# Kernel optimization log

Hardware: AMD Instinct MI355X
Metric: run time of the kernel (lower is better)

Reference implementation:

```python
import jax, jax.numpy as jnp
import numpy as np

N_NODES = 100000
N_EDGES = 1600000
IN_DIM, HID_DIM, N_CLASSES = 128, 64, 40


def spmm(edge_row, edge_col, edge_val, dense):
    # sparse [N,N] @ dense [N,D] via gather + segment-sum over edges
    msgs = edge_val[:, None] * dense[edge_col]            # [E, D]
    return jax.ops.segment_sum(msgs, edge_row, num_segments=N_NODES)


def setup_inputs() -> dict:
    key = jax.random.key(0)
    ks = jax.random.split(key, 8)
    x = jax.random.normal(ks[0], (N_NODES, IN_DIM), dtype=jnp.float32)
    edge_row = jax.random.randint(ks[1], (N_EDGES,), 0, N_NODES, dtype=jnp.int32)
    edge_col = jax.random.randint(ks[2], (N_EDGES,), 0, N_NODES, dtype=jnp.int32)
    edge_val = jax.random.uniform(ks[3], (N_EDGES,), dtype=jnp.float32)
    s1 = 1.0 / np.sqrt(IN_DIM)
    s2 = 1.0 / np.sqrt(HID_DIM)
    W1 = jax.random.normal(ks[4], (IN_DIM, HID_DIM), dtype=jnp.float32) * s1
    b1 = jnp.zeros((HID_DIM,), dtype=jnp.float32)
    W2 = jax.random.normal(ks[5], (HID_DIM, HID_DIM), dtype=jnp.float32) * s2
    b2 = jnp.zeros((HID_DIM,), dtype=jnp.float32)
    Wc = jax.random.normal(ks[6], (HID_DIM, N_CLASSES), dtype=jnp.float32) * s2
    bc = jnp.zeros((N_CLASSES,), dtype=jnp.float32)
    return {"x": x, "edge_row": edge_row, "edge_col": edge_col, "edge_val": edge_val,
            "W1": W1, "b1": b1, "W2": W2, "b2": b2, "Wc": Wc, "bc": bc}


def reference(x, edge_row, edge_col, edge_val, W1, b1, W2, b2, Wc, bc):
    # GCN layer 1: support = xW+b, aggregate, relu  (dropout off in eval)
    h = jax.nn.relu(spmm(edge_row, edge_col, edge_val, x @ W1 + b1))
    # GCN layer 2
    h = spmm(edge_row, edge_col, edge_val, h @ W2 + b2)
    # node classifier + log-softmax
    logits = h @ Wc + bc
    return jax.nn.log_softmax(logits, axis=-1)
```

## Files before the change

### kernel.cpp

```cpp
#include <hip/hip_runtime.h>

#define N_NODES   100000
#define N_EDGES   1600000
#define IN_DIM    128
#define HID_DIM   64
#define N_CLASSES 40

#define NBUCK 782
#define BCAP  2816
#define EPB   6400
#define PBLK  1024
#define GRID_A 250

typedef __attribute__((ext_vector_type(8))) short bf16x8;
typedef __attribute__((ext_vector_type(4))) float f32x4;

__device__ inline short f2bf(float f) {
    unsigned u = __float_as_uint(f);
    unsigned r = (u + 0x7FFFu + ((u >> 16) & 1u)) >> 16;
    return (short)r;
}
__device__ inline float bflo(unsigned w) { return __uint_as_float(w << 16); }
__device__ inline float bfhi(unsigned w) { return __uint_as_float(w & 0xFFFF0000u); }
__device__ inline float upval(unsigned w) { return __uint_as_float((w >> 17) << 16); }

__global__ __launch_bounds__(PBLK) void prep_parta(const int* __restrict__ erow,
                                                   const int* __restrict__ ecol,
                                                   const float* __restrict__ eval,
                                                   int* __restrict__ bcnt,
                                                   int2* __restrict__ tmp,
                                                   const float* __restrict__ W1,
                                                   const float* __restrict__ W2,
                                                   const float* __restrict__ Wc,
                                                   const float* __restrict__ b2,
                                                   short* __restrict__ W1t,
                                                   short* __restrict__ Mt,
                                                   float* __restrict__ bv) {
    __shared__ int2 pay[EPB];
    __shared__ int hist[NBUCK], lbase[NBUCK], cur[NBUCK], dofs[NBUCK], scan[NBUCK];
    int tid = threadIdx.x;
    if (blockIdx.x >= GRID_A) {
        int pb = blockIdx.x - GRID_A;
        {
            int i = pb * PBLK + tid;
            int n = i >> 7, k = i & 127;
            W1t[i] = f2bf(W1[k * HID_DIM + n]);
        }
        if (pb == 0) {
            for (int idx = tid; idx < HID_DIM * HID_DIM; idx += PBLK) {
                int n = idx >> 6, i = idx & 63;
                float acc = 0.f;
                if (n < N_CLASSES)
                    for (int j = 0; j < HID_DIM; ++j)
                        acc = fmaf(W2[i * HID_DIM + j], Wc[j * N_CLASSES + n], acc);
                Mt[n * HID_DIM + i] = f2bf(acc);
            }
        }
        if (pb == 1 && tid < N_CLASSES) {
            float acc = 0.f;
            for (int j = 0; j < HID_DIM; ++j)
                acc = fmaf(b2[j], Wc[j * N_CLASSES + tid], acc);
            bv[tid] = acc;
        }
        return;
    }
    int e0 = blockIdx.x * EPB;
    for (int i = tid; i < NBUCK; i += PBLK) { hist[i] = 0; cur[i] = 0; }
    __syncthreads();
    for (int i = tid; i < EPB; i += PBLK)
        atomicAdd(&hist[erow[e0 + i] >> 7], 1);
    __syncthreads();
    for (int i = tid; i < NBUCK; i += PBLK) {
        int n = hist[i];
        dofs[i] = i * BCAP + (n ? atomicAdd(&bcnt[i], n) : 0);
        scan[i] = n;
    }
    __syncthreads();
    for (int off = 1; off < NBUCK; off <<= 1) {
        int t = 0;
        if (tid < NBUCK && tid >= off) t = scan[tid - off];
        __syncthreads();
        if (tid < NBUCK) scan[tid] += t;
        __syncthreads();
    }
    if (tid < NBUCK) {
        lbase[tid] = scan[tid] - hist[tid];
        dofs[tid] -= lbase[tid];
    }
    __syncthreads();
    for (int i = tid; i < EPB; i += PBLK) {
        int e = e0 + i;
        int r = erow[e];
        int b = r >> 7;
        int p = lbase[b] + atomicAdd(&cur[b], 1);
        unsigned u = __float_as_uint(eval[e]);
        unsigned vb = ((u + 0x7FFFu + ((u >> 16) & 1u)) >> 16) & 0x7FFFu;
        pay[p] = make_int2(((r & 127) << 17) | ecol[e], (int)((vb << 10) | (unsigned)b));
    }
    __syncthreads();
    for (int p = tid; p < EPB; p += PBLK) {
        int2 v = pay[p];
        int b = (unsigned)v.y & 1023u;
        int dest = dofs[b] + p;
        if (dest < (b + 1) * BCAP)
            tmp[dest] = v;
    }
}

__global__ __launch_bounds__(256) void part_b_gemm1(const int* __restrict__ bcnt,
                                                    const int2* __restrict__ tmp,
                                                    unsigned* __restrict__ tmp2,
                                                    int2* __restrict__ rowmeta,
                                                    const float* __restrict__ x,
                                                    const short* __restrict__ W1t,
                                                    const float* __restrict__ b1,
                                                    unsigned short* __restrict__ outH) {
    __shared__ int2 ein[BCAP];
    __shared__ unsigned eout[BCAP];
    __shared__ int hist[128], pad[128], basep[128], cur[128], scan[128];
    if (blockIdx.x < NBUCK) {
        int b = blockIdx.x;
        int nb = bcnt[b]; if (nb > BCAP) nb = BCAP;
        for (int i = threadIdx.x; i < nb; i += 256) ein[i] = tmp[(size_t)b * BCAP + i];
        if (threadIdx.x < 128) { hist[threadIdx.x] = 0; cur[threadIdx.x] = 0; }
        __syncthreads();
        for (int i = threadIdx.x; i < nb; i += 256)
            atomicAdd(&hist[(ein[i].x >> 17) & 127], 1);
        __syncthreads();
        if (threadIdx.x < 128) {
            pad[threadIdx.x] = (hist[threadIdx.x] + 3) & ~3;
            scan[threadIdx.x] = pad[threadIdx.x];
        }
        __syncthreads();
        for (int off = 1; off < 128; off <<= 1) {
            int t = 0;
            if (threadIdx.x < 128 && threadIdx.x >= off) t = scan[threadIdx.x - off];
            __syncthreads();
            if (threadIdx.x < 128) scan[threadIdx.x] += t;
            __syncthreads();
        }
        if (threadIdx.x < 128) basep[threadIdx.x] = scan[threadIdx.x] - pad[threadIdx.x];
        __syncthreads();
        int ntot = scan[127]; if (ntot > BCAP) ntot = BCAP;
        for (int i = threadIdx.x; i < nb; i += 256) {
            int lr = (ein[i].x >> 17) & 127;
            int p = basep[lr] + atomicAdd(&cur[lr], 1);
            if (p < BCAP) {
                unsigned vb = ((unsigned)ein[i].y >> 10) & 0x7FFFu;
                eout[p] = (vb << 17) | (unsigned)(ein[i].x & 0x1FFFF);
            }
        }
        __syncthreads();
        if (threadIdx.x < 128) {
            int pe = basep[threadIdx.x] + pad[threadIdx.x];
            for (int p = basep[threadIdx.x] + hist[threadIdx.x]; p < pe && p < BCAP; ++p)
                eout[p] = 0u;
        }
        __syncthreads();
        for (int i = threadIdx.x; i < ntot; i += 256) tmp2[(size_t)b * BCAP + i] = eout[i];
        if (threadIdx.x < 128) {
            int r = b * 128 + threadIdx.x;
            if (r < N_NODES)
                rowmeta[r] = make_int2(b * BCAP + basep[threadIdx.x], pad[threadIdx.x]);
        }
    } else {
        int gb = blockIdx.x - NBUCK;
        int wave = threadIdx.x >> 6;
        int lane = threadIdx.x & 63;
        int node0 = gb * 64 + wave * 16;
        if (node0 >= N_NODES) return;
        int m = lane & 15;
        int q = lane >> 4;
        const float* xrow = x + (size_t)(node0 + m) * IN_DIM;
        f32x4 acc0 = {0,0,0,0}, acc1 = {0,0,0,0}, acc2 = {0,0,0,0}, acc3 = {0,0,0,0};
#pragma unroll
        for (int kb = 0; kb < 4; ++kb) {
            int k0 = kb * 32 + q * 8;
            float4 a0 = *(const float4*)(xrow + k0);
            float4 a1 = *(const float4*)(xrow + k0 + 4);
            bf16x8 af;
            af[0]=f2bf(a0.x); af[1]=f2bf(a0.y); af[2]=f2bf(a0.z); af[3]=f2bf(a0.w);
            af[4]=f2bf(a1.x); af[5]=f2bf(a1.y); af[6]=f2bf(a1.z); af[7]=f2bf(a1.w);
            bf16x8 bf0 = *(const bf16x8*)(W1t + ( 0 + m) * IN_DIM + k0);
            bf16x8 bf1 = *(const bf16x8*)(W1t + (16 + m) * IN_DIM + k0);
            bf16x8 bf2 = *(const bf16x8*)(W1t + (32 + m) * IN_DIM + k0);
            bf16x8 bf3 = *(const bf16x8*)(W1t + (48 + m) * IN_DIM + k0);
            acc0 = __builtin_amdgcn_mfma_f32_16x16x32_bf16(af, bf0, acc0, 0, 0, 0);
            acc1 = __builtin_amdgcn_mfma_f32_16x16x32_bf16(af, bf1, acc1, 0, 0, 0);
            acc2 = __builtin_amdgcn_mfma_f32_16x16x32_bf16(af, bf2, acc2, 0, 0, 0);
            acc3 = __builtin_amdgcn_mfma_f32_16x16x32_bf16(af, bf3, acc3, 0, 0, 0);
        }
        f32x4 accs[4] = {acc0, acc1, acc2, acc3};
#pragma unroll
        for (int t = 0; t < 4; ++t) {
            float bias = b1[t * 16 + m];
#pragma unroll
            for (int r = 0; r < 4; ++r) {
                int node = node0 + q * 4 + r;
                outH[(size_t)node * HID_DIM + t * 16 + m] = (unsigned short)f2bf(accs[t][r] + bias);
            }
        }
    }
}

__global__ __launch_bounds__(256) void spmm1_mm(const int2* __restrict__ rowmeta,
                                                const unsigned* __restrict__ ecv,
                                                const unsigned short* __restrict__ dense,
                                                const short* __restrict__ Mt,
                                                unsigned short* __restrict__ outU) {
    __shared__ unsigned lm[4][8][68];
    __shared__ unsigned short tr[32][64];
    int wave = threadIdx.x >> 6;
    int lane = threadIdx.x & 63;
    int s = lane >> 3, dq = lane & 7;
    int row = wave * 8 + s;
    int r = blockIdx.x * 32 + row;
    int2 meta = rowmeta[r];
    int beg = meta.x, deg = meta.y;
    int degc = deg < 64 ? deg : 64;
    for (int e = dq; e < degc; e += 8)
        lm[wave][s][e] = ecv[beg + e];
    __syncthreads();
    const unsigned* mp = lm[wave][s];
    float a0=0,a1=0,a2=0,a3=0,a4=0,a5=0,a6=0,a7=0;
    if (deg > 0) {
        uint4 w = *(const uint4*)mp;
        for (int e = 0; e < degc; e += 4) {
            uint4 wn = (e + 4 < degc) ? *(const uint4*)(mp + e + 4) : w;
            uint4 g0 = *(const uint4*)(dense + ((size_t)(w.x & 0x1FFFF) << 6) + (dq << 3));
            uint4 g1 = *(const uint4*)(dense + ((size_t)(w.y & 0x1FFFF) << 6) + (dq << 3));
            uint4 g2 = *(const uint4*)(dense + ((size_t)(w.z & 0x1FFFF) << 6) + (dq << 3));
            uint4 g3 = *(const uint4*)(dense + ((size_t)(w.w & 0x1FFFF) << 6) + (dq << 3));
            float v0 = upval(w.x), v1 = upval(w.y), v2 = upval(w.z), v3 = upval(w.w);
            a0=fmaf(v0,bflo(g0.x),a0); a1=fmaf(v0,bfhi(g0.x),a1); a2=fmaf(v0,bflo(g0.y),a2); a3=fmaf(v0,bfhi(g0.y),a3);
            a4=fmaf(v0,bflo(g0.z),a4); a5=fmaf(v0,bfhi(g0.z),a5); a6=fmaf(v0,bflo(g0.w),a6); a7=fmaf(v0,bfhi(g0.w),a7);
            a0=fmaf(v1,bflo(g1.x),a0); a1=fmaf(v1,bfhi(g1.x),a1); a2=fmaf(v1,bflo(g1.y),a2); a3=fmaf(v1,bfhi(g1.y),a3);
            a4=fmaf(v1,bflo(g1.z),a4); a5=fmaf(v1,bfhi(g1.z),a5); a6=fmaf(v1,bflo(g1.w),a6); a7=fmaf(v1,bfhi(g1.w),a7);
            a0=fmaf(v2,bflo(g2.x),a0); a1=fmaf(v2,bfhi(g2.x),a1); a2=fmaf(v2,bflo(g2.y),a2); a3=fmaf(v2,bfhi(g2.y),a3);
            a4=fmaf(v2,bflo(g2.z),a4); a5=fmaf(v2,bfhi(g2.z),a5); a6=fmaf(v2,bflo(g2.w),a6); a7=fmaf(v2,bfhi(g2.w),a7);
            a0=fmaf(v3,bflo(g3.x),a0); a1=fmaf(v3,bfhi(g3.x),a1); a2=fmaf(v3,bflo(g3.y),a2); a3=fmaf(v3,bfhi(g3.y),a3);
            a4=fmaf(v3,bflo(g3.z),a4); a5=fmaf(v3,bfhi(g3.z),a5); a6=fmaf(v3,bflo(g3.w),a6); a7=fmaf(v3,bfhi(g3.w),a7);
            w = wn;
        }
        for (int e = 64; e < deg; ++e) {
            unsigned we = ecv[beg + e];
            uint4 g = *(const uint4*)(dense + ((size_t)(we & 0x1FFFF) << 6) + (dq << 3));
            float v = upval(we);
            a0=fmaf(v,bflo(g.x),a0); a1=fmaf(v,bfhi(g.x),a1); a2=fmaf(v,bflo(g.y),a2); a3=fmaf(v,bfhi(g.y),a3);
            a4=fmaf(v,bflo(g.z),a4); a5=fmaf(v,bfhi(g.z),a5); a6=fmaf(v,bflo(g.w),a6); a7=fmaf(v,bfhi(g.w),a7);
        }
    }
    uint4 o;
    o.x = (unsigned short)f2bf(fmaxf(a0,0.f)) | ((unsigned)(unsigned short)f2bf(fmaxf(a1,0.f)) << 16);
    o.y = (unsigned short)f2bf(fmaxf(a2,0.f)) | ((unsigned)(unsigned short)f2bf(fmaxf(a3,0.f)) << 16);
    o.z = (unsigned short)f2bf(fmaxf(a4,0.f)) | ((unsigned)(unsigned short)f2bf(fmaxf(a5,0.f)) << 16);
    o.w = (unsigned short)f2bf(fmaxf(a6,0.f)) | ((unsigned)(unsigned short)f2bf(fmaxf(a7,0.f)) << 16);
    *(uint4*)(&tr[row][(dq ^ s) << 3]) = o;
    __syncthreads();
    int m = lane & 15;
    int q = lane >> 4;
    int nt = wave >> 1;
    int tb = (wave & 1) << 1;
    int arow = nt * 16 + m;
    f32x4 c0 = {0,0,0,0}, c1 = {0,0,0,0};
#pragma unroll
    for (int kb = 0; kb < 2; ++kb) {
        int ch = kb * 4 + q;
        bf16x8 af = *(const bf16x8*)(&tr[arow][(ch ^ (arow & 7)) << 3]);
        int k0 = kb * 32 + q * 8;
        bf16x8 bf0 = *(const bf16x8*)(Mt + ((tb + 0) * 16 + m) * HID_DIM + k0);
        bf16x8 bf1 = *(const bf16x8*)(Mt + ((tb + 1) * 16 + m) * HID_DIM + k0);
        c0 = __builtin_amdgcn_mfma_f32_16x16x32_bf16(af, bf0, c0, 0, 0, 0);
        c1 = __builtin_amdgcn_mfma_f32_16x16x32_bf16(af, bf1, c1, 0, 0, 0);
    }
#pragma unroll
    for (int rr = 0; rr < 4; ++rr) {
        int node = blockIdx.x * 32 + nt * 16 + q * 4 + rr;
        outU[(size_t)node * HID_DIM + (tb + 0) * 16 + m] = (unsigned short)f2bf(c0[rr]);
        outU[(size_t)node * HID_DIM + (tb + 1) * 16 + m] = (unsigned short)f2bf(c1[rr]);
    }
}

__global__ __launch_bounds__(256) void spmm_cls(const int2* __restrict__ rowmeta,
                                                const unsigned* __restrict__ ecv,
                                                const unsigned short* __restrict__ dense,
                                                const float* __restrict__ bv,
                                                const float* __restrict__ bc,
                                                float* __restrict__ outF) {
    __shared__ unsigned lm[4][8][68];
    int wave = threadIdx.x >> 6;
    int lane = threadIdx.x & 63;
    int s = lane >> 3, dq = lane & 7;
    int r = (blockIdx.x * 4 + wave) * 8 + s;
    float4 bv0 = {0,0,0,0}, bv1 = {0,0,0,0}, bc0 = {0,0,0,0}, bc1 = {0,0,0,0};
    if (dq < 5) {
        bv0 = *(const float4*)(bv + dq * 8);  bv1 = *(const float4*)(bv + dq * 8 + 4);
        bc0 = *(const float4*)(bc + dq * 8);  bc1 = *(const float4*)(bc + dq * 8 + 4);
    }
    int2 meta = rowmeta[r];
    int beg = meta.x, deg = meta.y;
    int degc = deg < 64 ? deg : 64;
    for (int e = dq; e < degc; e += 8)
        lm[wave][s][e] = ecv[beg + e];
    __syncthreads();
    const unsigned* mp = lm[wave][s];
    float a0=0,a1=0,a2=0,a3=0,a4=0,a5=0,a6=0,a7=0, asum=0;
    if (deg > 0) {
        uint4 w = *(const uint4*)mp;
        for (int e = 0; e < degc; e += 4) {
            uint4 wn = (e + 4 < degc) ? *(const uint4*)(mp + e + 4) : w;
            uint4 g0 = *(const uint4*)(dense + ((size_t)(w.x & 0x1FFFF) << 6) + (dq << 3));
            uint4 g1 = *(const uint4*)(dense + ((size_t)(w.y & 0x1FFFF) << 6) + (dq << 3));
            uint4 g2 = *(const uint4*)(dense + ((size_t)(w.z & 0x1FFFF) << 6) + (dq << 3));
            uint4 g3 = *(const uint4*)(dense + ((size_t)(w.w & 0x1FFFF) << 6) + (dq << 3));
            float v0 = upval(w.x), v1 = upval(w.y), v2 = upval(w.z), v3 = upval(w.w);
            asum += v0 + v1 + v2 + v3;
            a0=fmaf(v0,bflo(g0.x),a0); a1=fmaf(v0,bfhi(g0.x),a1); a2=fmaf(v0,bflo(g0.y),a2); a3=fmaf(v0,bfhi(g0.y),a3);
            a4=fmaf(v0,bflo(g0.z),a4); a5=fmaf(v0,bfhi(g0.z),a5); a6=fmaf(v0,bflo(g0.w),a6); a7=fmaf(v0,bfhi(g0.w),a7);
            a0=fmaf(v1,bflo(g1.x),a0); a1=fmaf(v1,bfhi(g1.x),a1); a2=fmaf(v1,bflo(g1.y),a2); a3=fmaf(v1,bfhi(g1.y),a3);
            a4=fmaf(v1,bflo(g1.z),a4); a5=fmaf(v1,bfhi(g1.z),a5); a6=fmaf(v1,bflo(g1.w),a6); a7=fmaf(v1,bfhi(g1.w),a7);
            a0=fmaf(v2,bflo(g2.x),a0); a1=fmaf(v2,bfhi(g2.x),a1); a2=fmaf(v2,bflo(g2.y),a2); a3=fmaf(v2,bfhi(g2.y),a3);
            a4=fmaf(v2,bflo(g2.z),a4); a5=fmaf(v2,bfhi(g2.z),a5); a6=fmaf(v2,bflo(g2.w),a6); a7=fmaf(v2,bfhi(g2.w),a7);
            a0=fmaf(v3,bflo(g3.x),a0); a1=fmaf(v3,bfhi(g3.x),a1); a2=fmaf(v3,bflo(g3.y),a2); a3=fmaf(v3,bfhi(g3.y),a3);
            a4=fmaf(v3,bflo(g3.z),a4); a5=fmaf(v3,bfhi(g3.z),a5); a6=fmaf(v3,bflo(g3.w),a6); a7=fmaf(v3,bfhi(g3.w),a7);
            w = wn;
        }
        for (int e = 64; e < deg; ++e) {
            unsigned we = ecv[beg + e];
            uint4 g = *(const uint4*)(dense + ((size_t)(we & 0x1FFFF) << 6) + (dq << 3));
            float v = upval(we);
            asum += v;
            a0=fmaf(v,bflo(g.x),a0); a1=fmaf(v,bfhi(g.x),a1); a2=fmaf(v,bflo(g.y),a2); a3=fmaf(v,bfhi(g.y),a3);
            a4=fmaf(v,bflo(g.z),a4); a5=fmaf(v,bfhi(g.z),a5); a6=fmaf(v,bflo(g.w),a6); a7=fmaf(v,bfhi(g.w),a7);
        }
    }
    float l0 = fmaf(asum, bv0.x, a0) + bc0.x;
    float l1 = fmaf(asum, bv0.y, a1) + bc0.y;
    float l2 = fmaf(asum, bv0.z, a2) + bc0.z;
    float l3 = fmaf(asum, bv0.w, a3) + bc0.w;
    float l4 = fmaf(asum, bv1.x, a4) + bc1.x;
    float l5 = fmaf(asum, bv1.y, a5) + bc1.y;
    float l6 = fmaf(asum, bv1.z, a6) + bc1.z;
    float l7 = fmaf(asum, bv1.w, a7) + bc1.w;
    float mx = -1e30f;
    if (dq < 5)
        mx = fmaxf(fmaxf(fmaxf(l0, l1), fmaxf(l2, l3)),
                   fmaxf(fmaxf(l4, l5), fmaxf(l6, l7)));
#pragma unroll
    for (int off = 1; off < 8; off <<= 1) mx = fmaxf(mx, __shfl_xor(mx, off));
    float ss = 0.f;
    if (dq < 5)
        ss = __expf(l0 - mx) + __expf(l1 - mx) + __expf(l2 - mx) + __expf(l3 - mx)
           + __expf(l4 - mx) + __expf(l5 - mx) + __expf(l6 - mx) + __expf(l7 - mx);
#pragma unroll
    for (int off = 1; off < 8; off <<= 1) ss += __shfl_xor(ss, off);
    float lse = mx + __logf(ss);
    if (dq < 5) {
        float4 o0 = {l0 - lse, l1 - lse, l2 - lse, l3 - lse};
        float4 o1 = {l4 - lse, l5 - lse, l6 - lse, l7 - lse};
        float* dst = outF + (size_t)r * N_CLASSES + dq * 8;
        *(float4*)(dst) = o0;
        *(float4*)(dst + 4) = o1;
    }
}

extern "C" void kernel_launch(void* const* d_in, const int* in_sizes, int n_in,
                              void* d_out, int out_size, void* d_ws, size_t ws_size,
                              hipStream_t stream) {
    const float* x    = (const float*)d_in[0];
    const int*   erow = (const int*)  d_in[1];
    const int*   ecol = (const int*)  d_in[2];
    const float* eval = (const float*)d_in[3];
    const float* W1   = (const float*)d_in[4];
    const float* b1   = (const float*)d_in[5];
    const float* W2   = (const float*)d_in[6];
    const float* b2   = (const float*)d_in[7];
    const float* Wc   = (const float*)d_in[8];
    const float* bc   = (const float*)d_in[9];
    float* out = (float*)d_out;

    char* ws = (char*)d_ws;
    size_t off = 0;
    auto alloc = [&](size_t bytes) { char* p = ws + off; off += (bytes + 255) & ~(size_t)255; return p; };
    unsigned short* bufA = (unsigned short*)alloc((size_t)N_NODES * HID_DIM * sizeof(short));
    unsigned short* bufB = (unsigned short*)alloc((size_t)N_NODES * HID_DIM * sizeof(short));
    int2*     tmp     = (int2*)    alloc((size_t)NBUCK * BCAP * sizeof(int2));
    unsigned* tmp2    = (unsigned*)alloc((size_t)NBUCK * BCAP * sizeof(unsigned));
    int2*     rowmeta = (int2*)    alloc((size_t)N_NODES * sizeof(int2));
    int*      bcnt    = (int*)     alloc(NBUCK * sizeof(int));
    short*    W1t     = (short*)   alloc((size_t)IN_DIM * HID_DIM * sizeof(short));
    short*    Mt      = (short*)   alloc((size_t)HID_DIM * HID_DIM * sizeof(short));
    float*    bv      = (float*)   alloc(64 * sizeof(float));

    const int tile_grid = (N_NODES + 63) / 64;
    const int spmm_grid = N_NODES / 32;

    hipMemsetAsync(bcnt, 0, NBUCK * sizeof(int), stream);
    prep_parta<<<GRID_A + 8, PBLK, 0, stream>>>(erow, ecol, eval, bcnt, tmp,
                                                W1, W2, Wc, b2, W1t, Mt, bv);
    part_b_gemm1<<<NBUCK + tile_grid, 256, 0, stream>>>(bcnt, tmp, tmp2, rowmeta,
                                                        x, W1t, b1, bufA);
    spmm1_mm<<<spmm_grid, 256, 0, stream>>>(rowmeta, tmp2, bufA, Mt, bufB);
    spmm_cls<<<spmm_grid, 256, 0, stream>>>(rowmeta, tmp2, bufB, bv, bc, out);
}
```

Before: 232.3 us.

## Pack second-layer intermediate to 40 columns and unroll SpMM gathers by eight

The intermediate buffer passed between the two SpMM kernels now holds 40 bf16 columns per node (80-byte rows) instead of 64, which matches the class count. This cuts the bytes written by spmm1_mm and the random gather traffic in spmm_cls. Both SpMM loops are also restructured to issue eight independent gathers per iteration, with a 4-edge prologue, so more loads are in flight. In exchange, the 80-byte row stride leaves gathered rows unaligned to 128 bytes, and lanes with dq>=5 redundantly load offset 0.

After: 217.0 us. 1.07x faster.

```diff
diff --git a/kernel.cpp b/kernel.cpp
--- a/kernel.cpp
+++ b/kernel.cpp
@@ -5,6 +5,7 @@
 #define IN_DIM    128
 #define HID_DIM   64
 #define N_CLASSES 40
+#define U_DIM     40
 
 #define NBUCK 782
 #define BCAP  2816
@@ -203,6 +204,10 @@
     }
 }
 
+#define FMA8(v,g) \
+    a0=fmaf(v,bflo(g.x),a0); a1=fmaf(v,bfhi(g.x),a1); a2=fmaf(v,bflo(g.y),a2); a3=fmaf(v,bfhi(g.y),a3); \
+    a4=fmaf(v,bflo(g.z),a4); a5=fmaf(v,bfhi(g.z),a5); a6=fmaf(v,bflo(g.w),a6); a7=fmaf(v,bfhi(g.w),a7);
+
 __global__ __launch_bounds__(256) void spmm1_mm(const int2* __restrict__ rowmeta,
                                                 const unsigned* __restrict__ ecv,
                                                 const unsigned short* __restrict__ dense,
@@ -224,30 +229,38 @@
     const unsigned* mp = lm[wave][s];
     float a0=0,a1=0,a2=0,a3=0,a4=0,a5=0,a6=0,a7=0;
     if (deg > 0) {
-        uint4 w = *(const uint4*)mp;
-        for (int e = 0; e < degc; e += 4) {
-            uint4 wn = (e + 4 < degc) ? *(const uint4*)(mp + e + 4) : w;
+        int e = 0;
+        if (degc & 4) {
+            uint4 w = *(const uint4*)mp;
             uint4 g0 = *(const uint4*)(dense + ((size_t)(w.x & 0x1FFFF) << 6) + (dq << 3));
             uint4 g1 = *(const uint4*)(dense + ((size_t)(w.y & 0x1FFFF) << 6) + (dq << 3));
             uint4 g2 = *(const uint4*)(dense + ((size_t)(w.z & 0x1FFFF) << 6) + (dq << 3));
             uint4 g3 = *(const uint4*)(dense + ((size_t)(w.w & 0x1FFFF) << 6) + (dq << 3));
             float v0 = upval(w.x), v1 = upval(w.y), v2 = upval(w.z), v3 = upval(w.w);
-            a0=fmaf(v0,bflo(g0.x),a0); a1=fmaf(v0,bfhi(g0.x),a1); a2=fmaf(v0,bflo(g0.y),a2); a3=fmaf(v0,bfhi(g0.y),a3);
-            a4=fmaf(v0,bflo(g0.z),a4); a5=fmaf(v0,bfhi(g0.z),a5); a6=fmaf(v0,bflo(g0.w),a6); a7=fmaf(v0,bfhi(g0.w),a7);
-            a0=fmaf(v1,bflo(g1.x),a0); a1=fmaf(v1,bfhi(g1.x),a1); a2=fmaf(v1,bflo(g1.y),a2); a3=fmaf(v1,bfhi(g1.y),a3);
-            a4=fmaf(v1,bflo(g1.z),a4); a5=fmaf(v1,bfhi(g1.z),a5); a6=fmaf(v1,bflo(g1.w),a6); a7=fmaf(v1,bfhi(g1.w),a7);
-            a0=fmaf(v2,bflo(g2.x),a0); a1=fmaf(v2,bfhi(g2.x),a1); a2=fmaf(v2,bflo(g2.y),a2); a3=fmaf(v2,bfhi(g2.y),a3);
-            a4=fmaf(v2,bflo(g2.z),a4); a5=fmaf(v2,bfhi(g2.z),a5); a6=fmaf(v2,bflo(g2.w),a6); a7=fmaf(v2,bfhi(g2.w),a7);
-            a0=fmaf(v3,bflo(g3.x),a0); a1=fmaf(v3,bfhi(g3.x),a1); a2=fmaf(v3,bflo(g3.y),a2); a3=fmaf(v3,bfhi(g3.y),a3);
-            a4=fmaf(v3,bflo(g3.z),a4); a5=fmaf(v3,bfhi(g3.z),a5); a6=fmaf(v3,bflo(g3.w),a6); a7=fmaf(v3,bfhi(g3.w),a7);
-            w = wn;
-        }
-        for (int e = 64; e < deg; ++e) {
-            unsigned we = ecv[beg + e];
+            FMA8(v0,g0); FMA8(v1,g1); FMA8(v2,g2); FMA8(v3,g3);
+            e = 4;
+        }
+        for (; e < degc; e += 8) {
+            uint4 wa = *(const uint4*)(mp + e);
+            uint4 wb = *(const uint4*)(mp + e + 4);
+            uint4 g0 = *(const uint4*)(dense + ((size_t)(wa.x & 0x1FFFF) << 6) + (dq << 3));
+            uint4 g1 = *(const uint4*)(dense + ((size_t)(wa.y & 0x1FFFF) << 6) + (dq << 3));
+            uint4 g2 = *(const uint4*)(dense + ((size_t)(wa.z & 0x1FFFF) << 6) + (dq << 3));
+            uint4 g3 = *(const uint4*)(dense + ((size_t)(wa.w & 0x1FFFF) << 6) + (dq << 3));
+            uint4 g4 = *(const uint4*)(dense + ((size_t)(wb.x & 0x1FFFF) << 6) + (dq << 3));
+            uint4 g5 = *(const uint4*)(dense + ((size_t)(wb.y & 0x1FFFF) << 6) + (dq << 3));
+            uint4 g6 = *(const uint4*)(dense + ((size_t)(wb.z & 0x1FFFF) << 6) + (dq << 3));
+            uint4 g7 = *(const uint4*)(dense + ((size_t)(wb.w & 0x1FFFF) << 6) + (dq << 3));
+            float v0 = upval(wa.x), v1 = upval(wa.y), v2 = upval(wa.z), v3 = upval(wa.w);
+            float v4 = upval(wb.x), v5 = upval(wb.y), v6 = upval(wb.z), v7 = upval(wb.w);
+            FMA8(v0,g0); FMA8(v1,g1); FMA8(v2,g2); FMA8(v3,g3);
+            FMA8(v4,g4); FMA8(v5,g5); FMA8(v6,g6); FMA8(v7,g7);
+        }
+        for (int e2 = 64; e2 < deg; ++e2) {
+            unsigned we = ecv[beg + e2];
             uint4 g = *(const uint4*)(dense + ((size_t)(we & 0x1FFFF) << 6) + (dq << 3));
             float v = upval(we);
-            a0=fmaf(v,bflo(g.x),a0); a1=fmaf(v,bfhi(g.x),a1); a2=fmaf(v,bflo(g.y),a2); a3=fmaf(v,bfhi(g.y),a3);
-            a4=fmaf(v,bflo(g.z),a4); a5=fmaf(v,bfhi(g.z),a5); a6=fmaf(v,bflo(g.w),a6); a7=fmaf(v,bfhi(g.w),a7);
+            FMA8(v,g);
         }
     }
     uint4 o;
@@ -276,8 +289,12 @@
 #pragma unroll
     for (int rr = 0; rr < 4; ++rr) {
         int node = blockIdx.x * 32 + nt * 16 + q * 4 + rr;
-        outU[(size_t)node * HID_DIM + (tb + 0) * 16 + m] = (unsigned short)f2bf(c0[rr]);
-        outU[(size_t)node * HID_DIM + (tb + 1) * 16 + m] = (unsigned short)f2bf(c1[rr]);
+        int col0 = tb * 16 + m;
+        int col1 = col0 + 16;
+        if (col0 < U_DIM)
+            outU[(size_t)node * U_DIM + col0] = (unsigned short)f2bf(c0[rr]);
+        if (col1 < U_DIM)
+            outU[(size_t)node * U_DIM + col1] = (unsigned short)f2bf(c1[rr]);
     }
 }
 
@@ -291,6 +308,7 @@
     int wave = threadIdx.x >> 6;
     int lane = threadIdx.x & 63;
     int s = lane >> 3, dq = lane & 7;
+    int dof = (dq < 5 ? dq : 0) << 3;
     int r = (blockIdx.x * 4 + wave) * 8 + s;
     float4 bv0 = {0,0,0,0}, bv1 = {0,0,0,0}, bc0 = {0,0,0,0}, bc1 = {0,0,0,0};
     if (dq < 5) {
@@ -306,32 +324,41 @@
     const unsigned* mp = lm[wave][s];
     float a0=0,a1=0,a2=0,a3=0,a4=0,a5=0,a6=0,a7=0, asum=0;
     if (deg > 0) {
-        uint4 w = *(const uint4*)mp;
-        for (int e = 0; e < degc; e += 4) {
-            uint4 wn = (e + 4 < degc) ? *(const uint4*)(mp + e + 4) : w;
-            uint4 g0 = *(const uint4*)(dense + ((size_t)(w.x & 0x1FFFF) << 6) + (dq << 3));
-            uint4 g1 = *(const uint4*)(dense + ((size_t)(w.y & 0x1FFFF) << 6) + (dq << 3));
-            uint4 g2 = *(const uint4*)(dense + ((size_t)(w.z & 0x1FFFF) << 6) + (dq << 3));
-            uint4 g3 = *(const uint4*)(dense + ((size_t)(w.w & 0x1FFFF) << 6) + (dq << 3));
+        int e = 0;
+        if (degc & 4) {
+            uint4 w = *(const uint4*)mp;
+            uint4 g0 = *(const uint4*)(dense + (size_t)(w.x & 0x1FFFF) * U_DIM + dof);
+            uint4 g1 = *(const uint4*)(dense + (size_t)(w.y & 0x1FFFF) * U_DIM + dof);
+            uint4 g2 = *(const uint4*)(dense + (size_t)(w.z & 0x1FFFF) * U_DIM + dof);
+            uint4 g3 = *(const uint4*)(dense + (size_t)(w.w & 0x1FFFF) * U_DIM + dof);
             float v0 = upval(w.x), v1 = upval(w.y), v2 = upval(w.z), v3 = upval(w.w);
             asum += v0 + v1 + v2 + v3;
-            a0=fmaf(v0,bflo(g0.x),a0); a1=fmaf(v0,bfhi(g0.x),a1); a2=fmaf(v0,bflo(g0.y),a2); a3=fmaf(v0,bfhi(g0.y),a3);
-            a4=fmaf(v0,bflo(g0.z),a4); a5=fmaf(v0,bfhi(g0.z),a5); a6=fmaf(v0,bflo(g0.w),a6); a7=fmaf(v0,bfhi(g0.w),a7);
-            a0=fmaf(v1,bflo(g1.x),a0); a1=fmaf(v1,bfhi(g1.x),a1); a2=fmaf(v1,bflo(g1.y),a2); a3=fmaf(v1,bfhi(g1.y),a3);
-            a4=fmaf(v1,bflo(g1.z),a4); a5=fmaf(v1,bfhi(g1.z),a5); a6=fmaf(v1,bflo(g1.w),a6); a7=fmaf(v1,bfhi(g1.w),a7);
-            a0=fmaf(v2,bflo(g2.x),a0); a1=fmaf(v2,bfhi(g2.x),a1); a2=fmaf(v2,bflo(g2.y),a2); a3=fmaf(v2,bfhi(g2.y),a3);
-            a4=fmaf(v2,bflo(g2.z),a4); a5=fmaf(v2,bfhi(g2.z),a5); a6=fmaf(v2,bflo(g2.w),a6); a7=fmaf(v2,bfhi(g2.w),a7);
-            a0=fmaf(v3,bflo(g3.x),a0); a1=fmaf(v3,bfhi(g3.x),a1); a2=fmaf(v3,bflo(g3.y),a2); a3=fmaf(v3,bfhi(g3.y),a3);
-            a4=fmaf(v3,bflo(g3.z),a4); a5=fmaf(v3,bfhi(g3.z),a5); a6=fmaf(v3,bflo(g3.w),a6); a7=fmaf(v3,bfhi(g3.w),a7);
-            w = wn;
-        }
-        for (int e = 64; e < deg; ++e) {
-            unsigned we = ecv[beg + e];
-            uint4 g = *(const uint4*)(dense + ((size_t)(we & 0x1FFFF) << 6) + (dq << 3));
+            FMA8(v0,g0); FMA8(v1,g1); FMA8(v2,g2); FMA8(v3,g3);
+            e = 4;
+        }
+        for (; e < degc; e += 8) {
+            uint4 wa = *(const uint4*)(mp + e);
+            uint4 wb = *(const uint4*)(mp + e + 4);
+            uint4 g0 = *(const uint4*)(dense + (size_t)(wa.x & 0x1FFFF) * U_DIM + dof);
+            uint4 g1 = *(const uint4*)(dense + (size_t)(wa.y & 0x1FFFF) * U_DIM + dof);
+            uint4 g2 = *(const uint4*)(dense + (size_t)(wa.z & 0x1FFFF) * U_DIM + dof);
+            uint4 g3 = *(const uint4*)(dense + (size_t)(wa.w & 0x1FFFF) * U_DIM + dof);
+            uint4 g4 = *(const uint4*)(dense + (size_t)(wb.x & 0x1FFFF) * U_DIM + dof);
+            uint4 g5 = *(const uint4*)(dense + (size_t)(wb.y & 0x1FFFF) * U_DIM + dof);
+            uint4 g6 = *(const uint4*)(dense + (size_t)(wb.z & 0x1FFFF) * U_DIM + dof);
+            uint4 g7 = *(const uint4*)(dense + (size_t)(wb.w & 0x1FFFF) * U_DIM + dof);
+            float v0 = upval(wa.x), v1 = upval(wa.y), v2 = upval(wa.z), v3 = upval(wa.w);
+            float v4 = upval(wb.x), v5 = upval(wb.y), v6 = upval(wb.z), v7 = upval(wb.w);
+            asum += v0 + v1 + v2 + v3 + v4 + v5 + v6 + v7;
+            FMA8(v0,g0); FMA8(v1,g1); FMA8(v2,g2); FMA8(v3,g3);
+            FMA8(v4,g4); FMA8(v5,g5); FMA8(v6,g6); FMA8(v7,g7);
+        }
+        for (int e2 = 64; e2 < deg; ++e2) {
+            unsigned we = ecv[beg + e2];
+            uint4 g = *(const uint4*)(dense + (size_t)(we & 0x1FFFF) * U_DIM + dof);
             float v = upval(we);
             asum += v;
-            a0=fmaf(v,bflo(g.x),a0); a1=fmaf(v,bfhi(g.x),a1); a2=fmaf(v,bflo(g.y),a2); a3=fmaf(v,bfhi(g.y),a3);
-            a4=fmaf(v,bflo(g.z),a4); a5=fmaf(v,bfhi(g.z),a5); a6=fmaf(v,bflo(g.w),a6); a7=fmaf(v,bfhi(g.w),a7);
+            FMA8(v,g);
         }
     }
     float l0 = fmaf(asum, bv0.x, a0) + bc0.x;
@@ -383,7 +410,7 @@
     size_t off = 0;
     auto alloc = [&](size_t bytes) { char* p = ws + off; off += (bytes + 255) & ~(size_t)255; return p; };
     unsigned short* bufA = (unsigned short*)alloc((size_t)N_NODES * HID_DIM * sizeof(short));
-    unsigned short* bufB = (unsigned short*)alloc((size_t)N_NODES * HID_DIM * sizeof(short));
+    unsigned short* bufB = (unsigned short*)alloc((size_t)N_NODES * U_DIM * sizeof(short));
     int2*     tmp     = (int2*)    alloc((size_t)NBUCK * BCAP * sizeof(int2));
     unsigned* tmp2    = (unsigned*)alloc((size_t)NBUCK * BCAP * sizeof(unsigned));
     int2*     rowmeta = (int2*)    alloc((size_t)N_NODES * sizeof(int2));
```
